# Optimization experiments

Hardware: AMD Instinct MI355X
Metric: run time of the kernel (lower is better)

## Reference

```python
import jax, jax.numpy as jnp
import numpy as np

NH = 16          # n_head
TAU = 2.0        # gumbel-softmax temperature
CLAMP = 40.0     # safe_clamp bound for float32
NEG = -1e9       # masking value


def setup_inputs() -> dict:
    key = jax.random.key(0)
    k0, k1, k2, k3 = jax.random.split(key, 4)
    B, T, E = 2, 2048, 1024
    hidden_states = jax.random.normal(k0, (B, T, E), jnp.float32)
    Wq = jax.random.normal(k1, (E, E), jnp.float32) / np.float32(np.sqrt(E))
    bq = jnp.zeros((E,), jnp.float32)
    Wk = jax.random.normal(k2, (E, E), jnp.float32) / np.float32(np.sqrt(E))
    bk = jnp.zeros((E,), jnp.float32)
    # pre-drawn uniform noise for gumbel sampling (replaces the torch data-seeded RNG)
    gumbel_u = jax.random.uniform(k3, (B, T, T), jnp.float32, 1e-6, 1.0 - 1e-6)
    causal_lengths = jnp.arange(T, dtype=jnp.int32)  # growing causal context
    return {"hidden_states": hidden_states, "Wq": Wq, "bq": bq,
            "Wk": Wk, "bk": bk, "gumbel_u": gumbel_u,
            "causal_lengths": causal_lengths}


def reference(hidden_states, Wq, bq, Wk, bk, gumbel_u, causal_lengths):
    B, T, E = hidden_states.shape
    dh = E // NH
    # q/k in-projections (v and out_proj are dead code in the original: attn_out is discarded)
    q = (hidden_states @ Wq.T + bq).reshape(B, T, NH, dh)
    k = (hidden_states @ Wk.T + bk).reshape(B, T, NH, dh)
    scores = jnp.einsum('bthd,bshd->bhts', q, k) / np.float32(np.sqrt(dh))
    # ragged causal mask: key position s is valid for query t iff s < causal_lengths[t]
    mask = jnp.arange(T, dtype=causal_lengths.dtype)[None, :] < causal_lengths[:, None]  # [T,S]
    scores = jnp.where(mask[None, None], scores, NEG)
    attn_w = jax.nn.softmax(scores, axis=-1).mean(axis=1)   # head-averaged weights [B,T,S]
    attn_w = jnp.clip(attn_w, -CLAMP, CLAMP)                 # safe_clamp
    # gumbel-softmax (soft, tau=TAU) restricted to the valid ragged context
    g = -jnp.log(-jnp.log(gumbel_u))
    logits = jnp.where(mask[None], (attn_w + g) / TAU, NEG)
    dw = jax.nn.softmax(logits, axis=-1)                     # [B,T,S]
    out = jnp.einsum('bts,bse->bte', dw, hidden_states)      # weighted sum of RAW hidden states
    valid = (causal_lengths > 0).astype(hidden_states.dtype) # length-0 steps output zeros
    return out * valid[None, :, None]
```

## Files before the change

kernel.cpp:

```cpp
#include <hip/hip_runtime.h>
#include <hip/hip_bf16.h>
#include <math.h>
#include <stdint.h>


#define B_   2
#define T_   2048
#define E_   1024
#define NH_  16
#define DH_  64
#define M_   (B_ * T_)
#define SCALE_ 0.125f

typedef __attribute__((ext_vector_type(8))) short bf16x8;
typedef __attribute__((ext_vector_type(4))) float f32x4;

__device__ __forceinline__ short f2bf(float x) {
  __hip_bfloat16 h = __float2bfloat16(x);
  return *reinterpret_cast<short*>(&h);
}
__device__ __forceinline__ float bf2f(short x) {
  __hip_bfloat16 h = *reinterpret_cast<__hip_bfloat16*>(&x);
  return __bfloat162float(h);
}
__device__ __forceinline__ void tri_decode(int idx, int& ti, int& si) {
  int t = (int)((sqrtf(8.0f * (float)idx + 1.0f) - 1.0f) * 0.5f);
  while ((t + 1) * (t + 2) / 2 <= idx) ++t;
  while (t * (t + 1) / 2 > idx) --t;
  ti = t;
  si = idx - t * (t + 1) / 2;
}

__global__ __launch_bounds__(256) void prep_hs(
    const float* __restrict__ hs, short* __restrict__ hs_hi,
    short* __restrict__ hsT_hi, short* __restrict__ hsT_lo)
{
  const int b = blockIdx.z;
  const int s0 = blockIdx.x * 64, e0 = blockIdx.y * 64;
  __shared__ float tile[64][65];
  const int tid = threadIdx.x;
  const int r = tid >> 4, c4 = (tid & 15) * 4;

  #pragma unroll
  for (int rr = 0; rr < 64; rr += 16) {
    const float4 v = *(const float4*)(hs + (size_t)(b * T_ + s0 + r + rr) * E_ + e0 + c4);
    ushort4 o;
    o.x = (unsigned short)f2bf(v.x); o.y = (unsigned short)f2bf(v.y);
    o.z = (unsigned short)f2bf(v.z); o.w = (unsigned short)f2bf(v.w);
    *(ushort4*)(hs_hi + (size_t)(b * T_ + s0 + r + rr) * E_ + e0 + c4) = o;
    tile[r + rr][c4 + 0] = v.x; tile[r + rr][c4 + 1] = v.y;
    tile[r + rr][c4 + 2] = v.z; tile[r + rr][c4 + 3] = v.w;
  }
  __syncthreads();
  #pragma unroll
  for (int rr = 0; rr < 64; rr += 16) {
    ushort4 oh, ol;
    #pragma unroll
    for (int j = 0; j < 4; ++j) {
      const float v = tile[c4 + j][r + rr];
      const short hi = f2bf(v);
      const short lo = f2bf(v - bf2f(hi));
      ((unsigned short*)&oh)[j] = (unsigned short)hi;
      ((unsigned short*)&ol)[j] = (unsigned short)lo;
    }
    const size_t dst = (size_t)(b * E_ + e0 + r + rr) * T_ + s0 + c4;
    *(ushort4*)(hsT_hi + dst) = oh;
    *(ushort4*)(hsT_lo + dst) = ol;
  }
}

__global__ __launch_bounds__(256) void cast_w(
    const float* __restrict__ Wq, const float* __restrict__ Wk,
    short* __restrict__ Wqb, short* __restrict__ Wkb)
{
  const size_t i = ((size_t)blockIdx.x * 256 + threadIdx.x) * 4;
  const float4 q = *(const float4*)(Wq + i);
  const float4 k = *(const float4*)(Wk + i);
  ushort4 oq, ok;
  oq.x = (unsigned short)f2bf(q.x); oq.y = (unsigned short)f2bf(q.y);
  oq.z = (unsigned short)f2bf(q.z); oq.w = (unsigned short)f2bf(q.w);
  ok.x = (unsigned short)f2bf(k.x); ok.y = (unsigned short)f2bf(k.y);
  ok.z = (unsigned short)f2bf(k.z); ok.w = (unsigned short)f2bf(k.w);
  *(ushort4*)(Wqb + i) = oq;
  *(ushort4*)(Wkb + i) = ok;
}

__global__ __launch_bounds__(256) void proj_mfma(
    const short* __restrict__ hsb,
    const short* __restrict__ Wqb, const short* __restrict__ Wkb,
    const float* __restrict__ bq, const float* __restrict__ bk,
    short* __restrict__ Qb, short* __restrict__ Kb)
{
  const int nt = blockIdx.x;
  const int m0 = blockIdx.y * 128;
  const bool isK = nt >= 8;
  const short* __restrict__ Wsel = isK ? Wkb : Wqb;
  const float* __restrict__ bsel = isK ? bk : bq;
  short* __restrict__ Csel = isK ? Kb : Qb;
  const int nb = (nt & 7) * 128;

  __shared__ __align__(16) unsigned short Asm[128][72];
  __shared__ __align__(16) unsigned short Bsm[128][72];

  const int tid = threadIdx.x;
  const int wid = tid >> 6, l = tid & 63;
  const int lg = l >> 4, li = l & 15;
  const int wm = (wid >> 1) * 64, wn = (wid & 1) * 64;
  const int srow = tid >> 1, shalf = (tid & 1) * 32;

  f32x4 acc[4][4];
  #pragma unroll
  for (int i = 0; i < 4; ++i)
    #pragma unroll
    for (int j = 0; j < 4; ++j) acc[i][j] = (f32x4){0.f, 0.f, 0.f, 0.f};

  for (int kt = 0; kt < E_; kt += 64) {
    const short* ga = hsb + (size_t)(m0 + srow) * E_ + kt + shalf;
    const short* gb = Wsel + (size_t)(nb + srow) * E_ + kt + shalf;
    bf16x8 a0 = *(const bf16x8*)(ga);      bf16x8 a1 = *(const bf16x8*)(ga + 8);
    bf16x8 a2 = *(const bf16x8*)(ga + 16); bf16x8 a3 = *(const bf16x8*)(ga + 24);
    bf16x8 b0 = *(const bf16x8*)(gb);      bf16x8 b1 = *(const bf16x8*)(gb + 8);
    bf16x8 b2 = *(const bf16x8*)(gb + 16); bf16x8 b3 = *(const bf16x8*)(gb + 24);
    __syncthreads();
    *(bf16x8*)&Asm[srow][shalf + 0]  = a0; *(bf16x8*)&Asm[srow][shalf + 8]  = a1;
    *(bf16x8*)&Asm[srow][shalf + 16] = a2; *(bf16x8*)&Asm[srow][shalf + 24] = a3;
    *(bf16x8*)&Bsm[srow][shalf + 0]  = b0; *(bf16x8*)&Bsm[srow][shalf + 8]  = b1;
    *(bf16x8*)&Bsm[srow][shalf + 16] = b2; *(bf16x8*)&Bsm[srow][shalf + 24] = b3;
    __syncthreads();
    #pragma unroll
    for (int kb = 0; kb < 2; ++kb) {
      bf16x8 af[4], bfv[4];
      #pragma unroll
      for (int i = 0; i < 4; ++i)
        af[i] = *(const bf16x8*)&Asm[wm + i * 16 + li][kb * 32 + lg * 8];
      #pragma unroll
      for (int j = 0; j < 4; ++j)
        bfv[j] = *(const bf16x8*)&Bsm[wn + j * 16 + li][kb * 32 + lg * 8];
      #pragma unroll
      for (int i = 0; i < 4; ++i)
        #pragma unroll
        for (int j = 0; j < 4; ++j)
          acc[i][j] = __builtin_amdgcn_mfma_f32_16x16x32_bf16(af[i], bfv[j], acc[i][j], 0, 0, 0);
    }
  }

  #pragma unroll
  for (int j = 0; j < 4; ++j) {
    const int n = nb + wn + j * 16 + li;
    const float bv = bsel[n];
    #pragma unroll
    for (int i = 0; i < 4; ++i) {
      #pragma unroll
      for (int r = 0; r < 4; ++r) {
        const int m = m0 + wm + i * 16 + lg * 4 + r;
        Csel[(size_t)m * E_ + n] = f2bf(acc[i][j][r] + bv);
      }
    }
  }
}

__global__ __launch_bounds__(256) void zpart_kernel(
    const short* __restrict__ Qb, const short* __restrict__ Kb,
    const int* __restrict__ clen, float* __restrict__ zs)
{
  const int bh = blockIdx.y;
  const int b = bh >> 4, h = bh & 15;
  int ti, si;
  tri_decode(blockIdx.x, ti, si);
  const int t0 = ti * 128, s0 = si * 128;
  const int tid = threadIdx.x;
  const int w = tid >> 6, l = tid & 63, lg = l >> 4, li = l & 15;
  const int wm = (w >> 1) * 64, wn = (w & 1) * 64;

  __shared__ __align__(16) unsigned short Qs[128][72];
  __shared__ __align__(16) unsigned short Ks[128][72];
  __shared__ int len_s[128];

  {
    const int row = tid >> 1, half = (tid & 1) * 32;
    const short* gq = Qb + (size_t)(b * T_ + t0 + row) * E_ + h * DH_ + half;
    const short* gk = Kb + (size_t)(b * T_ + s0 + row) * E_ + h * DH_ + half;
    *(bf16x8*)&Qs[row][half + 0]  = *(const bf16x8*)(gq + 0);
    *(bf16x8*)&Qs[row][half + 8]  = *(const bf16x8*)(gq + 8);
    *(bf16x8*)&Qs[row][half + 16] = *(const bf16x8*)(gq + 16);
    *(bf16x8*)&Qs[row][half + 24] = *(const bf16x8*)(gq + 24);
    *(bf16x8*)&Ks[row][half + 0]  = *(const bf16x8*)(gk + 0);
    *(bf16x8*)&Ks[row][half + 8]  = *(const bf16x8*)(gk + 8);
    *(bf16x8*)&Ks[row][half + 16] = *(const bf16x8*)(gk + 16);
    *(bf16x8*)&Ks[row][half + 24] = *(const bf16x8*)(gk + 24);
  }
  if (tid < 128) {
    int L = clen[t0 + tid];
    len_s[tid] = L < 0 ? 0 : (L > T_ ? T_ : L);
  }
  __syncthreads();

  f32x4 acc[4][4];
  #pragma unroll
  for (int i = 0; i < 4; ++i)
    #pragma unroll
    for (int j = 0; j < 4; ++j) acc[i][j] = (f32x4){0.f, 0.f, 0.f, 0.f};

  #pragma unroll
  for (int kb = 0; kb < 2; ++kb) {
    bf16x8 af[4], bfv[4];
    #pragma unroll
    for (int i = 0; i < 4; ++i)
      af[i] = *(const bf16x8*)&Qs[wm + i * 16 + li][kb * 32 + lg * 8];
    #pragma unroll
    for (int j = 0; j < 4; ++j)
      bfv[j] = *(const bf16x8*)&Ks[wn + j * 16 + li][kb * 32 + lg * 8];
    #pragma unroll
    for (int i = 0; i < 4; ++i)
      #pragma unroll
      for (int j = 0; j < 4; ++j)
        acc[i][j] = __builtin_amdgcn_mfma_f32_16x16x32_bf16(af[i], bfv[j], acc[i][j], 0, 0, 0);
  }

  float zp[4][4];
  #pragma unroll
  for (int i = 0; i < 4; ++i)
    #pragma unroll
    for (int r = 0; r < 4; ++r) zp[i][r] = 0.f;

  #pragma unroll
  for (int i = 0; i < 4; ++i) {
    int lenr[4];
    #pragma unroll
    for (int r = 0; r < 4; ++r) lenr[r] = len_s[wm + i * 16 + lg * 4 + r];
    #pragma unroll
    for (int j = 0; j < 4; ++j) {
      const int scol = s0 + wn + j * 16 + li;
      #pragma unroll
      for (int r = 0; r < 4; ++r)
        if (scol < lenr[r]) zp[i][r] += __expf(acc[i][j][r] * SCALE_);
    }
  }

  #pragma unroll
  for (int i = 0; i < 4; ++i)
    #pragma unroll
    for (int r = 0; r < 4; ++r) {
      float v = zp[i][r];
      v += __shfl_xor(v, 1); v += __shfl_xor(v, 2);
      v += __shfl_xor(v, 4); v += __shfl_xor(v, 8);
      if (li == 0 && v > 0.f)
        atomicAdd(&zs[(size_t)bh * T_ + t0 + wm + i * 16 + lg * 4 + r], v);
    }
}

__global__ __launch_bounds__(256) void elgen_kernel(
    const short* __restrict__ Qb, const short* __restrict__ Kb,
    const float* __restrict__ zs, const float* __restrict__ gum,
    const int* __restrict__ clen,
    short* __restrict__ ELh, short* __restrict__ ELl, float* __restrict__ Lws)
{
  const int b = blockIdx.y;
  int ti, si;
  tri_decode(blockIdx.x, ti, si);
  const int t0 = ti * 64, s0 = si * 64;
  const int tid = threadIdx.x;
  const int w = tid >> 6, l = tid & 63, lg = l >> 4, li = l & 15;
  const int wr = (w >> 1) * 32, wc = (w & 1) * 32;

  __shared__ __align__(16) unsigned short Qs[64][136];
  __shared__ __align__(16) unsigned short Ks[64][136];
  __shared__ float rz_s[16][64];
  __shared__ int len_s[64];

  if (tid < 64) {
    int L = clen[t0 + tid];
    len_s[tid] = L < 0 ? 0 : (L > T_ ? T_ : L);
  }
  #pragma unroll
  for (int q = 0; q < 4; ++q) {
    const int e = tid * 4 + q;
    const float zv = zs[(size_t)(b * NH_ + (e >> 6)) * T_ + t0 + (e & 63)];
    rz_s[e >> 6][e & 63] = (zv > 0.f) ? 1.f / zv : 0.f;
  }

  f32x4 aw[2][2];
  #pragma unroll
  for (int i = 0; i < 2; ++i)
    #pragma unroll
    for (int j = 0; j < 2; ++j) aw[i][j] = (f32x4){0.f, 0.f, 0.f, 0.f};

  const int srow = tid >> 2, sch = (tid & 3) * 32;

  for (int p = 0; p < 8; ++p) {
    __syncthreads();
    const short* gq = Qb + (size_t)(b * T_ + t0 + srow) * E_ + p * 128 + sch;
    const short* gk = Kb + (size_t)(b * T_ + s0 + srow) * E_ + p * 128 + sch;
    *(bf16x8*)&Qs[srow][sch + 0]  = *(const bf16x8*)(gq);
    *(bf16x8*)&Qs[srow][sch + 8]  = *(const bf16x8*)(gq + 8);
    *(bf16x8*)&Qs[srow][sch + 16] = *(const bf16x8*)(gq + 16);
    *(bf16x8*)&Qs[srow][sch + 24] = *(const bf16x8*)(gq + 24);
    *(bf16x8*)&Ks[srow][sch + 0]  = *(const bf16x8*)(gk);
    *(bf16x8*)&Ks[srow][sch + 8]  = *(const bf16x8*)(gk + 8);
    *(bf16x8*)&Ks[srow][sch + 16] = *(const bf16x8*)(gk + 16);
    *(bf16x8*)&Ks[srow][sch + 24] = *(const bf16x8*)(gk + 24);
    __syncthreads();

    f32x4 sc[2][2][2];
    #pragma unroll
    for (int h2 = 0; h2 < 2; ++h2)
      #pragma unroll
      for (int i = 0; i < 2; ++i)
        #pragma unroll
        for (int j = 0; j < 2; ++j) sc[h2][i][j] = (f32x4){0.f, 0.f, 0.f, 0.f};

    #pragma unroll
    for (int h2 = 0; h2 < 2; ++h2) {
      #pragma unroll
      for (int kb = 0; kb < 2; ++kb) {
        const int kc = h2 * 64 + kb * 32 + lg * 8;
        bf16x8 af[2], bfv[2];
        af[0] = *(const bf16x8*)&Qs[wr + li][kc];
        af[1] = *(const bf16x8*)&Qs[wr + 16 + li][kc];
        bfv[0] = *(const bf16x8*)&Ks[wc + li][kc];
        bfv[1] = *(const bf16x8*)&Ks[wc + 16 + li][kc];
        #pragma unroll
        for (int i = 0; i < 2; ++i)
          #pragma unroll
          for (int j = 0; j < 2; ++j)
            sc[h2][i][j] = __builtin_amdgcn_mfma_f32_16x16x32_bf16(af[i], bfv[j], sc[h2][i][j], 0, 0, 0);
      }
    }
    #pragma unroll
    for (int i = 0; i < 2; ++i) {
      float rz0[4], rz1[4];
      #pragma unroll
      for (int r = 0; r < 4; ++r) {
        rz0[r] = rz_s[2 * p][wr + i * 16 + lg * 4 + r];
        rz1[r] = rz_s[2 * p + 1][wr + i * 16 + lg * 4 + r];
      }
      #pragma unroll
      for (int j = 0; j < 2; ++j)
        #pragma unroll
        for (int r = 0; r < 4; ++r)
          aw[i][j][r] += __expf(sc[0][i][j][r] * SCALE_) * rz0[r] +
                         __expf(sc[1][i][j][r] * SCALE_) * rz1[r];
    }
  }

  #pragma unroll
  for (int i = 0; i < 2; ++i) {
    float lrow[4] = {0.f, 0.f, 0.f, 0.f};
    #pragma unroll
    for (int r = 0; r < 4; ++r) {
      const int tl = wr + i * 16 + lg * 4 + r;
      const int lenr = len_s[tl];
      const size_t grow = (size_t)(b * T_ + t0 + tl) * T_;
      #pragma unroll
      for (int j = 0; j < 2; ++j) {
        const int scol = s0 + wc + j * 16 + li;
        float e = 0.f;
        if (scol < lenr) {
          const float u = gum[grow + scol];
          const float g = -__logf(-__logf(u));
          e = expf((aw[i][j][r] * (1.f / NH_) + g) * 0.5f);
        }
        const short hi = f2bf(e);
        const short lo = f2bf(e - bf2f(hi));
        ELh[grow + scol] = hi;
        ELl[grow + scol] = lo;
        lrow[r] += e;
      }
    }
    #pragma unroll
    for (int r = 0; r < 4; ++r) {
      float v = lrow[r];
      v += __shfl_xor(v, 1); v += __shfl_xor(v, 2);
      v += __shfl_xor(v, 4); v += __shfl_xor(v, 8);
      if (li == 0 && v > 0.f)
        atomicAdd(&Lws[(size_t)(b * T_) + t0 + wr + i * 16 + lg * 4 + r], v);
    }
  }
}

__global__ __launch_bounds__(256) void out_mfma(
    const short* __restrict__ ELh, const short* __restrict__ ELl,
    const short* __restrict__ HTh, const short* __restrict__ HTl,
    const float* __restrict__ Lws, const int* __restrict__ clen,
    float* __restrict__ outp)
{
  const int e0 = blockIdx.x * 128;
  const int m0 = ((int)gridDim.y - 1 - (int)blockIdx.y) * 64;
  const int b = m0 >> 11;
  const int tl0 = m0 & (T_ - 1);
  const int tid = threadIdx.x;
  const int w = tid >> 6, l = tid & 63, lg = l >> 4, li = l & 15;
  const int wr = (w >> 1) * 32, wc = (w & 1) * 64;

  __shared__ __align__(16) unsigned short Ah[64][40], Al[64][40];
  __shared__ __align__(16) unsigned short Bh[128][40], Bl[128][40];
  __shared__ int smax_sh;

  if (tid == 0) smax_sh = 0;
  __syncthreads();
  if (tid < 64) {
    int L = clen[tl0 + tid];
    L = L < 0 ? 0 : (L > T_ ? T_ : L);
    atomicMax(&smax_sh, L);
  }
  __syncthreads();
  const int kend = (smax_sh + 31) & ~31;

  const int ar = tid >> 2, ac = (tid & 3) * 8;
  const int br = tid >> 1, bc = (tid & 1) * 16;

  f32x4 acc[2][4];
  #pragma unroll
  for (int i = 0; i < 2; ++i)
    #pragma unroll
    for (int j = 0; j < 4; ++j) acc[i][j] = (f32x4){0.f, 0.f, 0.f, 0.f};

  for (int s0 = 0; s0 < kend; s0 += 32) {
    const size_t asrc = (size_t)(m0 + ar) * T_ + s0 + ac;
    const size_t bsrc = (size_t)(b * E_ + e0 + br) * T_ + s0 + bc;
    const bf16x8 vah  = *(const bf16x8*)(ELh + asrc);
    const bf16x8 val  = *(const bf16x8*)(ELl + asrc);
    const bf16x8 vbh0 = *(const bf16x8*)(HTh + bsrc);
    const bf16x8 vbh1 = *(const bf16x8*)(HTh + bsrc + 8);
    const bf16x8 vbl0 = *(const bf16x8*)(HTl + bsrc);
    const bf16x8 vbl1 = *(const bf16x8*)(HTl + bsrc + 8);
    __syncthreads();
    *(bf16x8*)&Ah[ar][ac] = vah;
    *(bf16x8*)&Al[ar][ac] = val;
    *(bf16x8*)&Bh[br][bc] = vbh0; *(bf16x8*)&Bh[br][bc + 8] = vbh1;
    *(bf16x8*)&Bl[br][bc] = vbl0; *(bf16x8*)&Bl[br][bc + 8] = vbl1;
    __syncthreads();
    bf16x8 ah[2], al[2], bh[4], bl[4];
    #pragma unroll
    for (int i = 0; i < 2; ++i) {
      ah[i] = *(const bf16x8*)&Ah[wr + i * 16 + li][lg * 8];
      al[i] = *(const bf16x8*)&Al[wr + i * 16 + li][lg * 8];
    }
    #pragma unroll
    for (int j = 0; j < 4; ++j) {
      bh[j] = *(const bf16x8*)&Bh[wc + j * 16 + li][lg * 8];
      bl[j] = *(const bf16x8*)&Bl[wc + j * 16 + li][lg * 8];
    }
    #pragma unroll
    for (int i = 0; i < 2; ++i)
      #pragma unroll
      for (int j = 0; j < 4; ++j) {
        acc[i][j] = __builtin_amdgcn_mfma_f32_16x16x32_bf16(ah[i], bh[j], acc[i][j], 0, 0, 0);
        acc[i][j] = __builtin_amdgcn_mfma_f32_16x16x32_bf16(ah[i], bl[j], acc[i][j], 0, 0, 0);
        acc[i][j] = __builtin_amdgcn_mfma_f32_16x16x32_bf16(al[i], bh[j], acc[i][j], 0, 0, 0);
      }
  }

  #pragma unroll
  for (int i = 0; i < 2; ++i)
    #pragma unroll
    for (int r = 0; r < 4; ++r) {
      const int m = m0 + wr + i * 16 + lg * 4 + r;
      const float Lv = Lws[m];
      const float inv = (Lv > 0.f) ? 1.f / Lv : 0.f;
      #pragma unroll
      for (int j = 0; j < 4; ++j)
        outp[(size_t)m * E_ + e0 + wc + j * 16 + li] = acc[i][j][r] * inv;
    }
}

extern "C" void kernel_launch(void* const* d_in, const int* in_sizes, int n_in,
                              void* d_out, int out_size, void* d_ws, size_t ws_size,
                              hipStream_t stream) {
  const float* hs  = (const float*)d_in[0];
  const float* Wq  = (const float*)d_in[1];
  const float* bq  = (const float*)d_in[2];
  const float* Wk  = (const float*)d_in[3];
  const float* bk  = (const float*)d_in[4];
  const float* gum = (const float*)d_in[5];
  const int*   cl  = (const int*)d_in[6];
  float* out = (float*)d_out;

  short* hs_hi  = (short*)d_ws;
  short* hsT_hi = hs_hi  + (size_t)M_ * E_;
  short* hsT_lo = hsT_hi + (size_t)B_ * E_ * T_;
  short* Wqb    = hsT_lo + (size_t)B_ * E_ * T_;
  short* Wkb    = Wqb + (size_t)E_ * E_;
  short* Qb     = Wkb + (size_t)E_ * E_;
  short* Kb     = Qb + (size_t)M_ * E_;
  short* ELh    = Kb + (size_t)M_ * E_;
  short* ELl    = ELh + (size_t)M_ * T_;
  float* zsws   = (float*)(ELl + (size_t)M_ * T_);
  float* Lw     = zsws + (size_t)B_ * NH_ * T_;
  (void)ws_size; (void)in_sizes; (void)n_in; (void)out_size;

  hipMemsetAsync(zsws, 0, (size_t)B_ * NH_ * T_ * sizeof(float), stream);
  hipMemsetAsync(Lw, 0, (size_t)M_ * sizeof(float), stream);
  prep_hs<<<dim3(T_ / 64, E_ / 64, B_), 256, 0, stream>>>(hs, hs_hi, hsT_hi, hsT_lo);
  cast_w<<<dim3((E_ * E_) / (256 * 4)), 256, 0, stream>>>(Wq, Wk, Wqb, Wkb);
  proj_mfma<<<dim3(16, M_ / 128), 256, 0, stream>>>(hs_hi, Wqb, Wkb, bq, bk, Qb, Kb);
  zpart_kernel<<<dim3(136, B_ * NH_), 256, 0, stream>>>(Qb, Kb, cl, zsws);
  elgen_kernel<<<dim3(528, B_), 256, 0, stream>>>(Qb, Kb, zsws, gum, cl, ELh, ELl, Lw);
  out_mfma<<<dim3(E_ / 128, M_ / 64), 256, 0, stream>>>(
      ELh, ELl, hsT_hi, hsT_lo, Lw, cl, out);
}
```

Before: 300.0 us.

## Switch pipeline from split-bf16 to single fp16 operands and retile output GEMM

Replaces bf16 storage and MFMA everywhere with fp16, and drops the hi/lo bf16 split used for the exp-weights and transposed hidden states. The output GEMM now runs one MFMA per tile instead of three, reads half the bytes of EL and hsT, and uses a 64x64 tile with a 64-wide k step. This cuts the output GEMM's memory traffic and matrix work, and also cuts the elgen and prep writes. The cost is precision: fp16 has an 11-bit mantissa, which is less than the roughly 16 bits the split-bf16 scheme gave. It also has a narrower range, so the unnormalized exp values must stay within fp16 limits.

```diff
diff --git a/kernel.cpp b/kernel.cpp
--- a/kernel.cpp
+++ b/kernel.cpp
@@ -12,16 +12,15 @@
 #define M_   (B_ * T_)
 #define SCALE_ 0.125f
 
-typedef __attribute__((ext_vector_type(8))) short bf16x8;
+typedef __attribute__((ext_vector_type(8))) _Float16 f16x8;
 typedef __attribute__((ext_vector_type(4))) float f32x4;
 
-__device__ __forceinline__ short f2bf(float x) {
-  __hip_bfloat16 h = __float2bfloat16(x);
+__device__ __forceinline__ short f2h(float x) {
+  _Float16 h = (_Float16)x;
   return *reinterpret_cast<short*>(&h);
 }
-__device__ __forceinline__ float bf2f(short x) {
-  __hip_bfloat16 h = *reinterpret_cast<__hip_bfloat16*>(&x);
-  return __bfloat162float(h);
+__device__ __forceinline__ float h2f(short s) {
+  return (float)(*reinterpret_cast<_Float16*>(&s));
 }
 __device__ __forceinline__ void tri_decode(int idx, int& ti, int& si) {
   int t = (int)((sqrtf(8.0f * (float)idx + 1.0f) - 1.0f) * 0.5f);
@@ -32,8 +31,8 @@
 }
 
 __global__ __launch_bounds__(256) void prep_hs(
-    const float* __restrict__ hs, short* __restrict__ hs_hi,
-    short* __restrict__ hsT_hi, short* __restrict__ hsT_lo)
+    const float* __restrict__ hs, short* __restrict__ hs16,
+    short* __restrict__ hsT16)
 {
   const int b = blockIdx.z;
   const int s0 = blockIdx.x * 64, e0 = blockIdx.y * 64;
@@ -45,58 +44,51 @@
   for (int rr = 0; rr < 64; rr += 16) {
     const float4 v = *(const float4*)(hs + (size_t)(b * T_ + s0 + r + rr) * E_ + e0 + c4);
     ushort4 o;
-    o.x = (unsigned short)f2bf(v.x); o.y = (unsigned short)f2bf(v.y);
-    o.z = (unsigned short)f2bf(v.z); o.w = (unsigned short)f2bf(v.w);
-    *(ushort4*)(hs_hi + (size_t)(b * T_ + s0 + r + rr) * E_ + e0 + c4) = o;
+    o.x = (unsigned short)f2h(v.x); o.y = (unsigned short)f2h(v.y);
+    o.z = (unsigned short)f2h(v.z); o.w = (unsigned short)f2h(v.w);
+    *(ushort4*)(hs16 + (size_t)(b * T_ + s0 + r + rr) * E_ + e0 + c4) = o;
     tile[r + rr][c4 + 0] = v.x; tile[r + rr][c4 + 1] = v.y;
     tile[r + rr][c4 + 2] = v.z; tile[r + rr][c4 + 3] = v.w;
   }
   __syncthreads();
   #pragma unroll
   for (int rr = 0; rr < 64; rr += 16) {
-    ushort4 oh, ol;
-    #pragma unroll
-    for (int j = 0; j < 4; ++j) {
-      const float v = tile[c4 + j][r + rr];
-      const short hi = f2bf(v);
-      const short lo = f2bf(v - bf2f(hi));
-      ((unsigned short*)&oh)[j] = (unsigned short)hi;
-      ((unsigned short*)&ol)[j] = (unsigned short)lo;
-    }
-    const size_t dst = (size_t)(b * E_ + e0 + r + rr) * T_ + s0 + c4;
-    *(ushort4*)(hsT_hi + dst) = oh;
-    *(ushort4*)(hsT_lo + dst) = ol;
+    ushort4 o;
+    #pragma unroll
+    for (int j = 0; j < 4; ++j)
+      ((unsigned short*)&o)[j] = (unsigned short)f2h(tile[c4 + j][r + rr]);
+    *(ushort4*)(hsT16 + (size_t)(b * E_ + e0 + r + rr) * T_ + s0 + c4) = o;
   }
 }
 
 __global__ __launch_bounds__(256) void cast_w(
     const float* __restrict__ Wq, const float* __restrict__ Wk,
-    short* __restrict__ Wqb, short* __restrict__ Wkb)
+    short* __restrict__ Wq16, short* __restrict__ Wk16)
 {
   const size_t i = ((size_t)blockIdx.x * 256 + threadIdx.x) * 4;
   const float4 q = *(const float4*)(Wq + i);
   const float4 k = *(const float4*)(Wk + i);
   ushort4 oq, ok;
-  oq.x = (unsigned short)f2bf(q.x); oq.y = (unsigned short)f2bf(q.y);
-  oq.z = (unsigned short)f2bf(q.z); oq.w = (unsigned short)f2bf(q.w);
-  ok.x = (unsigned short)f2bf(k.x); ok.y = (unsigned short)f2bf(k.y);
-  ok.z = (unsigned short)f2bf(k.z); ok.w = (unsigned short)f2bf(k.w);
-  *(ushort4*)(Wqb + i) = oq;
-  *(ushort4*)(Wkb + i) = ok;
+  oq.x = (unsigned short)f2h(q.x); oq.y = (unsigned short)f2h(q.y);
+  oq.z = (unsigned short)f2h(q.z); oq.w = (unsigned short)f2h(q.w);
+  ok.x = (unsigned short)f2h(k.x); ok.y = (unsigned short)f2h(k.y);
+  ok.z = (unsigned short)f2h(k.z); ok.w = (unsigned short)f2h(k.w);
+  *(ushort4*)(Wq16 + i) = oq;
+  *(ushort4*)(Wk16 + i) = ok;
 }
 
 __global__ __launch_bounds__(256) void proj_mfma(
     const short* __restrict__ hsb,
-    const short* __restrict__ Wqb, const short* __restrict__ Wkb,
+    const short* __restrict__ Wq16, const short* __restrict__ Wk16,
     const float* __restrict__ bq, const float* __restrict__ bk,
-    short* __restrict__ Qb, short* __restrict__ Kb)
+    short* __restrict__ Qh, short* __restrict__ Kh)
 {
   const int nt = blockIdx.x;
   const int m0 = blockIdx.y * 128;
   const bool isK = nt >= 8;
-  const short* __restrict__ Wsel = isK ? Wkb : Wqb;
+  const short* __restrict__ Wsel = isK ? Wk16 : Wq16;
   const float* __restrict__ bsel = isK ? bk : bq;
-  short* __restrict__ Csel = isK ? Kb : Qb;
+  short* __restrict__ Csel = isK ? Kh : Qh;
   const int nb = (nt & 7) * 128;
 
   __shared__ __align__(16) unsigned short Asm[128][72];
@@ -117,30 +109,30 @@
   for (int kt = 0; kt < E_; kt += 64) {
     const short* ga = hsb + (size_t)(m0 + srow) * E_ + kt + shalf;
     const short* gb = Wsel + (size_t)(nb + srow) * E_ + kt + shalf;
-    bf16x8 a0 = *(const bf16x8*)(ga);      bf16x8 a1 = *(const bf16x8*)(ga + 8);
-    bf16x8 a2 = *(const bf16x8*)(ga + 16); bf16x8 a3 = *(const bf16x8*)(ga + 24);
-    bf16x8 b0 = *(const bf16x8*)(gb);      bf16x8 b1 = *(const bf16x8*)(gb + 8);
-    bf16x8 b2 = *(const bf16x8*)(gb + 16); bf16x8 b3 = *(const bf16x8*)(gb + 24);
-    __syncthreads();
-    *(bf16x8*)&Asm[srow][shalf + 0]  = a0; *(bf16x8*)&Asm[srow][shalf + 8]  = a1;
-    *(bf16x8*)&Asm[srow][shalf + 16] = a2; *(bf16x8*)&Asm[srow][shalf + 24] = a3;
-    *(bf16x8*)&Bsm[srow][shalf + 0]  = b0; *(bf16x8*)&Bsm[srow][shalf + 8]  = b1;
-    *(bf16x8*)&Bsm[srow][shalf + 16] = b2; *(bf16x8*)&Bsm[srow][shalf + 24] = b3;
+    f16x8 a0 = *(const f16x8*)(ga);      f16x8 a1 = *(const f16x8*)(ga + 8);
+    f16x8 a2 = *(const f16x8*)(ga + 16); f16x8 a3 = *(const f16x8*)(ga + 24);
+    f16x8 b0 = *(const f16x8*)(gb);      f16x8 b1 = *(const f16x8*)(gb + 8);
+    f16x8 b2 = *(const f16x8*)(gb + 16); f16x8 b3 = *(const f16x8*)(gb + 24);
+    __syncthreads();
+    *(f16x8*)&Asm[srow][shalf + 0]  = a0; *(f16x8*)&Asm[srow][shalf + 8]  = a1;
+    *(f16x8*)&Asm[srow][shalf + 16] = a2; *(f16x8*)&Asm[srow][shalf + 24] = a3;
+    *(f16x8*)&Bsm[srow][shalf + 0]  = b0; *(f16x8*)&Bsm[srow][shalf + 8]  = b1;
+    *(f16x8*)&Bsm[srow][shalf + 16] = b2; *(f16x8*)&Bsm[srow][shalf + 24] = b3;
     __syncthreads();
     #pragma unroll
     for (int kb = 0; kb < 2; ++kb) {
-      bf16x8 af[4], bfv[4];
+      f16x8 af[4], bfv[4];
       #pragma unroll
       for (int i = 0; i < 4; ++i)
-        af[i] = *(const bf16x8*)&Asm[wm + i * 16 + li][kb * 32 + lg * 8];
+        af[i] = *(const f16x8*)&Asm[wm + i * 16 + li][kb * 32 + lg * 8];
       #pragma unroll
       for (int j = 0; j < 4; ++j)
-        bfv[j] = *(const bf16x8*)&Bsm[wn + j * 16 + li][kb * 32 + lg * 8];
+        bfv[j] = *(const f16x8*)&Bsm[wn + j * 16 + li][kb * 32 + lg * 8];
       #pragma unroll
       for (int i = 0; i < 4; ++i)
         #pragma unroll
         for (int j = 0; j < 4; ++j)
-          acc[i][j] = __builtin_amdgcn_mfma_f32_16x16x32_bf16(af[i], bfv[j], acc[i][j], 0, 0, 0);
+          acc[i][j] = __builtin_amdgcn_mfma_f32_16x16x32_f16(af[i], bfv[j], acc[i][j], 0, 0, 0);
     }
   }
 
@@ -153,14 +145,14 @@
       #pragma unroll
       for (int r = 0; r < 4; ++r) {
         const int m = m0 + wm + i * 16 + lg * 4 + r;
-        Csel[(size_t)m * E_ + n] = f2bf(acc[i][j][r] + bv);
+        Csel[(size_t)m * E_ + n] = f2h(acc[i][j][r] + bv);
       }
     }
   }
 }
 
 __global__ __launch_bounds__(256) void zpart_kernel(
-    const short* __restrict__ Qb, const short* __restrict__ Kb,
+    const short* __restrict__ Qh, const short* __restrict__ Kh,
     const int* __restrict__ clen, float* __restrict__ zs)
 {
   const int bh = blockIdx.y;
@@ -178,16 +170,16 @@
 
   {
     const int row = tid >> 1, half = (tid & 1) * 32;
-    const short* gq = Qb + (size_t)(b * T_ + t0 + row) * E_ + h * DH_ + half;
-    const short* gk = Kb + (size_t)(b * T_ + s0 + row) * E_ + h * DH_ + half;
-    *(bf16x8*)&Qs[row][half + 0]  = *(const bf16x8*)(gq + 0);
-    *(bf16x8*)&Qs[row][half + 8]  = *(const bf16x8*)(gq + 8);
-    *(bf16x8*)&Qs[row][half + 16] = *(const bf16x8*)(gq + 16);
-    *(bf16x8*)&Qs[row][half + 24] = *(const bf16x8*)(gq + 24);
-    *(bf16x8*)&Ks[row][half + 0]  = *(const bf16x8*)(gk + 0);
-    *(bf16x8*)&Ks[row][half + 8]  = *(const bf16x8*)(gk + 8);
-    *(bf16x8*)&Ks[row][half + 16] = *(const bf16x8*)(gk + 16);
-    *(bf16x8*)&Ks[row][half + 24] = *(const bf16x8*)(gk + 24);
+    const short* gq = Qh + (size_t)(b * T_ + t0 + row) * E_ + h * DH_ + half;
+    const short* gk = Kh + (size_t)(b * T_ + s0 + row) * E_ + h * DH_ + half;
+    *(f16x8*)&Qs[row][half + 0]  = *(const f16x8*)(gq + 0);
+    *(f16x8*)&Qs[row][half + 8]  = *(const f16x8*)(gq + 8);
+    *(f16x8*)&Qs[row][half + 16] = *(const f16x8*)(gq + 16);
+    *(f16x8*)&Qs[row][half + 24] = *(const f16x8*)(gq + 24);
+    *(f16x8*)&Ks[row][half + 0]  = *(const f16x8*)(gk + 0);
+    *(f16x8*)&Ks[row][half + 8]  = *(const f16x8*)(gk + 8);
+    *(f16x8*)&Ks[row][half + 16] = *(const f16x8*)(gk + 16);
+    *(f16x8*)&Ks[row][half + 24] = *(const f16x8*)(gk + 24);
   }
   if (tid < 128) {
     int L = clen[t0 + tid];
@@ -203,18 +195,18 @@
 
   #pragma unroll
   for (int kb = 0; kb < 2; ++kb) {
-    bf16x8 af[4], bfv[4];
+    f16x8 af[4], bfv[4];
     #pragma unroll
     for (int i = 0; i < 4; ++i)
-      af[i] = *(const bf16x8*)&Qs[wm + i * 16 + li][kb * 32 + lg * 8];
+      af[i] = *(const f16x8*)&Qs[wm + i * 16 + li][kb * 32 + lg * 8];
     #pragma unroll
     for (int j = 0; j < 4; ++j)
-      bfv[j] = *(const bf16x8*)&Ks[wn + j * 16 + li][kb * 32 + lg * 8];
+      bfv[j] = *(const f16x8*)&Ks[wn + j * 16 + li][kb * 32 + lg * 8];
     #pragma unroll
     for (int i = 0; i < 4; ++i)
       #pragma unroll
       for (int j = 0; j < 4; ++j)
-        acc[i][j] = __builtin_amdgcn_mfma_f32_16x16x32_bf16(af[i], bfv[j], acc[i][j], 0, 0, 0);
+        acc[i][j] = __builtin_amdgcn_mfma_f32_16x16x32_f16(af[i], bfv[j], acc[i][j], 0, 0, 0);
   }
 
   float zp[4][4];
@@ -250,10 +242,10 @@
 }
 
 __global__ __launch_bounds__(256) void elgen_kernel(
-    const short* __restrict__ Qb, const short* __restrict__ Kb,
+    const short* __restrict__ Qh, const short* __restrict__ Kh,
     const float* __restrict__ zs, const float* __restrict__ gum,
     const int* __restrict__ clen,
-    short* __restrict__ ELh, short* __restrict__ ELl, float* __restrict__ Lws)
+    short* __restrict__ EL, float* __restrict__ Lws)
 {
   const int b = blockIdx.y;
   int ti, si;
@@ -289,16 +281,16 @@
 
   for (int p = 0; p < 8; ++p) {
     __syncthreads();
-    const short* gq = Qb + (size_t)(b * T_ + t0 + srow) * E_ + p * 128 + sch;
-    const short* gk = Kb + (size_t)(b * T_ + s0 + srow) * E_ + p * 128 + sch;
-    *(bf16x8*)&Qs[srow][sch + 0]  = *(const bf16x8*)(gq);
-    *(bf16x8*)&Qs[srow][sch + 8]  = *(const bf16x8*)(gq + 8);
-    *(bf16x8*)&Qs[srow][sch + 16] = *(const bf16x8*)(gq + 16);
-    *(bf16x8*)&Qs[srow][sch + 24] = *(const bf16x8*)(gq + 24);
-    *(bf16x8*)&Ks[srow][sch + 0]  = *(const bf16x8*)(gk);
-    *(bf16x8*)&Ks[srow][sch + 8]  = *(const bf16x8*)(gk + 8);
-    *(bf16x8*)&Ks[srow][sch + 16] = *(const bf16x8*)(gk + 16);
-    *(bf16x8*)&Ks[srow][sch + 24] = *(const bf16x8*)(gk + 24);
+    const short* gq = Qh + (size_t)(b * T_ + t0 + srow) * E_ + p * 128 + sch;
+    const short* gk = Kh + (size_t)(b * T_ + s0 + srow) * E_ + p * 128 + sch;
+    *(f16x8*)&Qs[srow][sch + 0]  = *(const f16x8*)(gq);
+    *(f16x8*)&Qs[srow][sch + 8]  = *(const f16x8*)(gq + 8);
+    *(f16x8*)&Qs[srow][sch + 16] = *(const f16x8*)(gq + 16);
+    *(f16x8*)&Qs[srow][sch + 24] = *(const f16x8*)(gq + 24);
+    *(f16x8*)&Ks[srow][sch + 0]  = *(const f16x8*)(gk);
+    *(f16x8*)&Ks[srow][sch + 8]  = *(const f16x8*)(gk + 8);
+    *(f16x8*)&Ks[srow][sch + 16] = *(const f16x8*)(gk + 16);
+    *(f16x8*)&Ks[srow][sch + 24] = *(const f16x8*)(gk + 24);
     __syncthreads();
 
     f32x4 sc[2][2][2];
@@ -314,16 +306,16 @@
       #pragma unroll
       for (int kb = 0; kb < 2; ++kb) {
         const int kc = h2 * 64 + kb * 32 + lg * 8;
-        bf16x8 af[2], bfv[2];
-        af[0] = *(const bf16x8*)&Qs[wr + li][kc];
-        af[1] = *(const bf16x8*)&Qs[wr + 16 + li][kc];
-        bfv[0] = *(const bf16x8*)&Ks[wc + li][kc];
-        bfv[1] = *(const bf16x8*)&Ks[wc + 16 + li][kc];
+        f16x8 af[2], bfv[2];
+        af[0] = *(const f16x8*)&Qs[wr + li][kc];
+        af[1] = *(const f16x8*)&Qs[wr + 16 + li][kc];
+        bfv[0] = *(const f16x8*)&Ks[wc + li][kc];
+        bfv[1] = *(const f16x8*)&Ks[wc + 16 + li][kc];
         #pragma unroll
         for (int i = 0; i < 2; ++i)
           #pragma unroll
           for (int j = 0; j < 2; ++j)
-            sc[h2][i][j] = __builtin_amdgcn_mfma_f32_16x16x32_bf16(af[i], bfv[j], sc[h2][i][j], 0, 0, 0);
+            sc[h2][i][j] = __builtin_amdgcn_mfma_f32_16x16x32_f16(af[i], bfv[j], sc[h2][i][j], 0, 0, 0);
       }
     }
     #pragma unroll
@@ -360,10 +352,7 @@
           const float g = -__logf(-__logf(u));
           e = expf((aw[i][j][r] * (1.f / NH_) + g) * 0.5f);
         }
-        const short hi = f2bf(e);
-        const short lo = f2bf(e - bf2f(hi));
-        ELh[grow + scol] = hi;
-        ELl[grow + scol] = lo;
+        EL[grow + scol] = f2h(e);
         lrow[r] += e;
       }
     }
@@ -379,21 +368,19 @@
 }
 
 __global__ __launch_bounds__(256) void out_mfma(
-    const short* __restrict__ ELh, const short* __restrict__ ELl,
-    const short* __restrict__ HTh, const short* __restrict__ HTl,
+    const short* __restrict__ EL, const short* __restrict__ HT,
     const float* __restrict__ Lws, const int* __restrict__ clen,
     float* __restrict__ outp)
 {
-  const int e0 = blockIdx.x * 128;
+  const int e0 = blockIdx.x * 64;
   const int m0 = ((int)gridDim.y - 1 - (int)blockIdx.y) * 64;
   const int b = m0 >> 11;
   const int tl0 = m0 & (T_ - 1);
   const int tid = threadIdx.x;
   const int w = tid >> 6, l = tid & 63, lg = l >> 4, li = l & 15;
-  const int wr = (w >> 1) * 32, wc = (w & 1) * 64;
-
-  __shared__ __align__(16) unsigned short Ah[64][40], Al[64][40];
-  __shared__ __align__(16) unsigned short Bh[128][40], Bl[128][40];
+
+  __shared__ __align__(16) unsigned short As[64][72];
+  __shared__ __align__(16) unsigned short Bs[64][72];
   __shared__ int smax_sh;
 
   if (tid == 0) smax_sh = 0;
@@ -404,64 +391,47 @@
     atomicMax(&smax_sh, L);
   }
   __syncthreads();
-  const int kend = (smax_sh + 31) & ~31;
-
-  const int ar = tid >> 2, ac = (tid & 3) * 8;
-  const int br = tid >> 1, bc = (tid & 1) * 16;
-
-  f32x4 acc[2][4];
-  #pragma unroll
-  for (int i = 0; i < 2; ++i)
-    #pragma unroll
-    for (int j = 0; j < 4; ++j) acc[i][j] = (f32x4){0.f, 0.f, 0.f, 0.f};
-
-  for (int s0 = 0; s0 < kend; s0 += 32) {
-    const size_t asrc = (size_t)(m0 + ar) * T_ + s0 + ac;
-    const size_t bsrc = (size_t)(b * E_ + e0 + br) * T_ + s0 + bc;
-    const bf16x8 vah  = *(const bf16x8*)(ELh + asrc);
-    const bf16x8 val  = *(const bf16x8*)(ELl + asrc);
-    const bf16x8 vbh0 = *(const bf16x8*)(HTh + bsrc);
-    const bf16x8 vbh1 = *(const bf16x8*)(HTh + bsrc + 8);
-    const bf16x8 vbl0 = *(const bf16x8*)(HTl + bsrc);
-    const bf16x8 vbl1 = *(const bf16x8*)(HTl + bsrc + 8);
-    __syncthreads();
-    *(bf16x8*)&Ah[ar][ac] = vah;
-    *(bf16x8*)&Al[ar][ac] = val;
-    *(bf16x8*)&Bh[br][bc] = vbh0; *(bf16x8*)&Bh[br][bc + 8] = vbh1;
-    *(bf16x8*)&Bl[br][bc] = vbl0; *(bf16x8*)&Bl[br][bc + 8] = vbl1;
-    __syncthreads();
-    bf16x8 ah[2], al[2], bh[4], bl[4];
-    #pragma unroll
-    for (int i = 0; i < 2; ++i) {
-      ah[i] = *(const bf16x8*)&Ah[wr + i * 16 + li][lg * 8];
-      al[i] = *(const bf16x8*)&Al[wr + i * 16 + li][lg * 8];
-    }
-    #pragma unroll
-    for (int j = 0; j < 4; ++j) {
-      bh[j] = *(const bf16x8*)&Bh[wc + j * 16 + li][lg * 8];
-      bl[j] = *(const bf16x8*)&Bl[wc + j * 16 + li][lg * 8];
-    }
-    #pragma unroll
-    for (int i = 0; i < 2; ++i)
-      #pragma unroll
-      for (int j = 0; j < 4; ++j) {
-        acc[i][j] = __builtin_amdgcn_mfma_f32_16x16x32_bf16(ah[i], bh[j], acc[i][j], 0, 0, 0);
-        acc[i][j] = __builtin_amdgcn_mfma_f32_16x16x32_bf16(ah[i], bl[j], acc[i][j], 0, 0, 0);
-        acc[i][j] = __builtin_amdgcn_mfma_f32_16x16x32_bf16(al[i], bh[j], acc[i][j], 0, 0, 0);
-      }
-  }
-
-  #pragma unroll
-  for (int i = 0; i < 2; ++i)
-    #pragma unroll
-    for (int r = 0; r < 4; ++r) {
-      const int m = m0 + wr + i * 16 + lg * 4 + r;
-      const float Lv = Lws[m];
-      const float inv = (Lv > 0.f) ? 1.f / Lv : 0.f;
+  const int kend = (smax_sh + 63) & ~63;
+
+  const int srow = tid >> 2, sc16 = (tid & 3) * 16;
+
+  f32x4 acc[4];
+  #pragma unroll
+  for (int j = 0; j < 4; ++j) acc[j] = (f32x4){0.f, 0.f, 0.f, 0.f};
+
+  for (int s0 = 0; s0 < kend; s0 += 64) {
+    const size_t asrc = (size_t)(m0 + srow) * T_ + s0 + sc16;
+    const size_t bsrc = (size_t)(b * E_ + e0 + srow) * T_ + s0 + sc16;
+    const f16x8 va0 = *(const f16x8*)(EL + asrc);
+    const f16x8 va1 = *(const f16x8*)(EL + asrc + 8);
+    const f16x8 vb0 = *(const f16x8*)(HT + bsrc);
+    const f16x8 vb1 = *(const f16x8*)(HT + bsrc + 8);
+    __syncthreads();
+    *(f16x8*)&As[srow][sc16] = va0; *(f16x8*)&As[srow][sc16 + 8] = va1;
+    *(f16x8*)&Bs[srow][sc16] = vb0; *(f16x8*)&Bs[srow][sc16 + 8] = vb1;
+    __syncthreads();
+    #pragma unroll
+    for (int kb = 0; kb < 2; ++kb) {
+      const f16x8 af = *(const f16x8*)&As[w * 16 + li][kb * 32 + lg * 8];
+      f16x8 bfv[4];
       #pragma unroll
       for (int j = 0; j < 4; ++j)
-        outp[(size_t)m * E_ + e0 + wc + j * 16 + li] = acc[i][j][r] * inv;
-    }
+        bfv[j] = *(const f16x8*)&Bs[j * 16 + li][kb * 32 + lg * 8];
+      #pragma unroll
+      for (int j = 0; j < 4; ++j)
+        acc[j] = __builtin_amdgcn_mfma_f32_16x16x32_f16(af, bfv[j], acc[j], 0, 0, 0);
+    }
+  }
+
+  #pragma unroll
+  for (int r = 0; r < 4; ++r) {
+    const int m = m0 + w * 16 + lg * 4 + r;
+    const float Lv = Lws[m];
+    const float inv = (Lv > 0.f) ? 1.f / Lv : 0.f;
+    #pragma unroll
+    for (int j = 0; j < 4; ++j)
+      outp[(size_t)m * E_ + e0 + j * 16 + li] = acc[j][r] * inv;
+  }
 }
 
 extern "C" void kernel_launch(void* const* d_in, const int* in_sizes, int n_in,
@@ -476,26 +446,23 @@
   const int*   cl  = (const int*)d_in[6];
   float* out = (float*)d_out;
 
-  short* hs_hi  = (short*)d_ws;
-  short* hsT_hi = hs_hi  + (size_t)M_ * E_;
-  short* hsT_lo = hsT_hi + (size_t)B_ * E_ * T_;
-  short* Wqb    = hsT_lo + (size_t)B_ * E_ * T_;
-  short* Wkb    = Wqb + (size_t)E_ * E_;
-  short* Qb     = Wkb + (size_t)E_ * E_;
-  short* Kb     = Qb + (size_t)M_ * E_;
-  short* ELh    = Kb + (size_t)M_ * E_;
-  short* ELl    = ELh + (size_t)M_ * T_;
-  float* zsws   = (float*)(ELl + (size_t)M_ * T_);
-  float* Lw     = zsws + (size_t)B_ * NH_ * T_;
+  short* hs16  = (short*)d_ws;
+  short* hsT16 = hs16  + (size_t)M_ * E_;
+  short* Wq16  = hsT16 + (size_t)B_ * E_ * T_;
+  short* Wk16  = Wq16 + (size_t)E_ * E_;
+  short* Qh    = Wk16 + (size_t)E_ * E_;
+  short* Kh    = Qh + (size_t)M_ * E_;
+  short* ELws  = Kh + (size_t)M_ * E_;
+  float* zsws  = (float*)(ELws + (size_t)M_ * T_);
+  float* Lw    = zsws + (size_t)B_ * NH_ * T_;
   (void)ws_size; (void)in_sizes; (void)n_in; (void)out_size;
 
   hipMemsetAsync(zsws, 0, (size_t)B_ * NH_ * T_ * sizeof(float), stream);
   hipMemsetAsync(Lw, 0, (size_t)M_ * sizeof(float), stream);
-  prep_hs<<<dim3(T_ / 64, E_ / 64, B_), 256, 0, stream>>>(hs, hs_hi, hsT_hi, hsT_lo);
-  cast_w<<<dim3((E_ * E_) / (256 * 4)), 256, 0, stream>>>(Wq, Wk, Wqb, Wkb);
-  proj_mfma<<<dim3(16, M_ / 128), 256, 0, stream>>>(hs_hi, Wqb, Wkb, bq, bk, Qb, Kb);
-  zpart_kernel<<<dim3(136, B_ * NH_), 256, 0, stream>>>(Qb, Kb, cl, zsws);
-  elgen_kernel<<<dim3(528, B_), 256, 0, stream>>>(Qb, Kb, zsws, gum, cl, ELh, ELl, Lw);
-  out_mfma<<<dim3(E_ / 128, M_ / 64), 256, 0, stream>>>(
-      ELh, ELl, hsT_hi, hsT_lo, Lw, cl, out);
-}
+  prep_hs<<<dim3(T_ / 64, E_ / 64, B_), 256, 0, stream>>>(hs, hs16, hsT16);
+  cast_w<<<dim3((E_ * E_) / (256 * 4)), 256, 0, stream>>>(Wq, Wk, Wq16, Wk16);
+  proj_mfma<<<dim3(16, M_ / 128), 256, 0, stream>>>(hs16, Wq16, Wk16, bq, bk, Qh, Kh);
+  zpart_kernel<<<dim3(136, B_ * NH_), 256, 0, stream>>>(Qh, Kh, cl, zsws);
+  elgen_kernel<<<dim3(528, B_), 256, 0, stream>>>(Qh, Kh, zsws, gum, cl, ELws, Lw);
+  out_mfma<<<dim3(E_ / 64, M_ / 64), 256, 0, stream>>>(ELws, hsT16, Lw, cl, out);
+}
```

Result: faster. 256.4 us (-14.5%).
